# Performance work log

Measured on AMD Instinct MI355X. Metric: run time of the kernel, lower is better.

## Reference

```python
import jax, jax.numpy as jnp
import numpy as np

CC_ITERS = 60  # min-label propagation + pointer doubling; covers huge diameters


def setup_inputs() -> dict:
    key = jax.random.key(0)
    k1, k2, k3, k4, k5 = jax.random.split(key, 5)
    N, C, E = 100000, 128, 800000
    x = jax.random.normal(k1, (N, C), jnp.float32)
    src = jax.random.randint(k2, (E,), 0, N)
    off = jax.random.randint(k3, (E,), 1, N)
    dst = (src + off) % N  # guarantees no self-loops (torch forward filters them)
    edge_index = jnp.stack([src, dst]).astype(jnp.int32)
    batch = jnp.zeros((N,), jnp.int32)
    W = jax.random.normal(k4, (2 * C,), jnp.float32) * 0.05
    b = (jax.random.normal(k5, (), jnp.float32) * 0.05).astype(jnp.float32)
    return {"x": x, "edge_index": edge_index, "batch": batch, "W": W, "b": b}


def _connected_components(src, dst, mask, N):
    # min-label propagation along selected edges, with path compression.
    def body(i, labels):
        ls = jnp.where(mask, labels[src], N)
        ld = jnp.where(mask, labels[dst], N)
        new = labels.at[dst].min(ls).at[src].min(ld)
        return jnp.minimum(new, new[new])  # pointer doubling
    return jax.lax.fori_loop(0, CC_ITERS, body, jnp.arange(N))


def reference(x, edge_index, batch, W, b):
    N, C = x.shape
    E = edge_index.shape[1]
    src, dst = edge_index[0], edge_index[1]

    # raw edge score: Linear(cat(x[src], x[dst])) without materializing the concat
    e = x[src] @ W[:C] + x[dst] @ W[C:] + b  # [E]
    # softmax over incoming edges of each dst node (segment softmax)
    m = jax.ops.segment_max(e, dst, num_segments=N)
    z = jnp.exp(e - m[dst])
    s = jax.ops.segment_sum(z, dst, num_segments=N)
    score = z / s[dst] + 0.5  # add_to_edge_score

    # edge selection (E > N -> quantile branch, matching torch)
    if E > N:
        q = 1.0 - (N // 2) / E
        mask = score > jnp.quantile(score, q)
    else:
        mask = score >= jnp.median(score)

    # weighted pairwise node reps for selected edges (masked instead of gathered)
    w = jnp.where(mask, score, 0.0)
    reps = (x[src] + x[dst]) * w[:, None]  # [E, C]
    mi = mask.astype(x.dtype)
    cnt = jnp.zeros((N,), x.dtype).at[src].add(mi).at[dst].add(mi)  # bincount of selected endpoints
    merged = cnt > 0
    base = jnp.where(merged[:, None], 0.0, x)  # merged nodes zeroed, untouched nodes keep x
    acc = base.at[src].add(reps).at[dst].add(reps)
    nodes = jnp.where(merged[:, None], acc / jnp.maximum(cnt, 1.0)[:, None], acc)

    # connected components over selected edges; relabel by first-occurrence order
    labels = _connected_components(src, dst, jax.lax.stop_gradient(mask), N)
    uniq = jnp.unique(labels, size=N, fill_value=N)
    cluster = jnp.searchsorted(uniq, labels)  # [N]

    new_x = jax.ops.segment_sum(nodes, cluster, num_segments=N)  # padded to N clusters

    # coalesce cluster-mapped edges: sorted unique pairs, padded with -1
    c0, c1 = cluster[src], cluster[dst]
    keys = jnp.unique(c0.astype(jnp.int64) * N + c1.astype(jnp.int64), size=E, fill_value=-1)
    valid = keys >= 0
    new_edge_index = jnp.stack([
        jnp.where(valid, keys // N, -1),
        jnp.where(valid, keys % N, -1),
    ])
    new_batch = jnp.zeros((N,), batch.dtype).at[cluster].set(batch)
    return new_x, new_edge_index, new_batch, score
```

## Files before the change

### kernel.cpp

```cpp
#include <hip/hip_runtime.h>
#include <math.h>
#include <stdint.h>

typedef unsigned long long u64;
typedef unsigned int u32;

#define NN 100000
#define CF 128
#define EE 800000

#define CAP 131072

#define EBITS 11
#define ERADIX 2048
#define STILE 2048
#define NB_E 391
#define SORT_N (NB_E * STILE)
#define MBITS 12
#define MRADIX 4096
#define NB_M 49
#define MSORT_N (NB_M * STILE)
#define HISTG_LEN 800768

#define SCTILE 2048
#define MCHUNK 16

#define ZSCALE 4503599627370496.0
#define XSCALE 32768.0f
#define XINV   (1.0f / 32768.0f)

struct Sel { u32 prefix; u32 k; };

__device__ inline u64 encD(double v) {
  u64 u = (u64)__double_as_longlong(v);
  return u ^ ((u >> 63) ? ~0ULL : 0x8000000000000000ULL);
}
__device__ inline double decD(u64 u) {
  u ^= ((u >> 63) ? 0x8000000000000000ULL : ~0ULL);
  return __longlong_as_double((long long)u);
}

__global__ void k_pq(const float* __restrict__ x, const float* __restrict__ W,
                     double* __restrict__ p, double* __restrict__ q) {
  int node = blockIdx.x * 4 + (threadIdx.x >> 6);
  int lane = threadIdx.x & 63;
  if (node >= NN) return;
  const float* xr = x + (size_t)node * CF;
  double a = (double)xr[lane] * (double)W[lane] + (double)xr[lane + 64] * (double)W[lane + 64];
  double c = (double)xr[lane] * (double)W[CF + lane] + (double)xr[lane + 64] * (double)W[CF + lane + 64];
  for (int off = 32; off; off >>= 1) { a += __shfl_xor(a, off); c += __shfl_xor(c, off); }
  if (lane == 0) { p[node] = a; q[node] = c; }
}

__global__ void k_em(const int* __restrict__ ei, const double* __restrict__ p,
                     const double* __restrict__ q, const float* __restrict__ bptr,
                     double* __restrict__ e, u64* __restrict__ menc) {
  int j = blockIdx.x * 256 + threadIdx.x;
  if (j >= EE) return;
  int s = ei[j], d = ei[EE + j];
  double ev = p[s] + q[d] + (double)bptr[0];
  e[j] = ev;
  atomicMax(&menc[d], encD(ev));
}

__global__ void k_zs(const int* __restrict__ ei, double* __restrict__ e,
                     const u64* __restrict__ menc, u64* __restrict__ sdenFx) {
  int j = blockIdx.x * 256 + threadIdx.x;
  if (j >= EE) return;
  int d = ei[EE + j];
  double z = exp(e[j] - decD(menc[d]));
  e[j] = z;
  atomicAdd(&sdenFx[d], (u64)__double2ll_rn(z * ZSCALE));
}

__global__ void k_score(const int* __restrict__ ei, const double* __restrict__ z,
                        const u64* __restrict__ sdenFx, float* __restrict__ outScore) {
  int j = blockIdx.x * 256 + threadIdx.x;
  if (j >= EE) return;
  int d = ei[EE + j];
  double s = (double)sdenFx[d] * (1.0 / ZSCALE);
  outScore[j] = (float)(z[j] / s + 0.5);
}

__global__ void k_selInit(Sel* st, u32* hist, int k0, int k1) {
  int t = blockIdx.x * 256 + threadIdx.x;
  if (t == 0) { st[0].prefix = 0; st[0].k = (u32)k0; st[1].prefix = 0; st[1].k = (u32)k1; }
  if (t < 512) hist[t] = 0;
}

__global__ void k_selHist(const float* __restrict__ score, const Sel* __restrict__ st,
                          u32* __restrict__ hist, int shift, int pass) {
  __shared__ u32 h[512];
  for (int i = threadIdx.x; i < 512; i += 256) h[i] = 0;
  __syncthreads();
  u32 p0 = st[0].prefix, p1 = st[1].prefix;
  for (int j = blockIdx.x * 256 + threadIdx.x; j < EE; j += gridDim.x * 256) {
    u32 u = __float_as_uint(score[j]);
    u32 d = (u >> shift) & 255u;
    bool ok0 = (pass == 0) || ((u >> (shift + 8)) == p0);
    bool ok1 = (pass == 0) || ((u >> (shift + 8)) == p1);
    if (ok0) atomicAdd(&h[d], 1u);
    if (ok1) atomicAdd(&h[256 + d], 1u);
  }
  __syncthreads();
  for (int i = threadIdx.x; i < 512; i += 256) if (h[i]) atomicAdd(&hist[i], h[i]);
}

__global__ void k_selPick(Sel* st, u32* hist) {
  if (threadIdx.x == 0) {
    for (int sel = 0; sel < 2; sel++) {
      u32 k = st[sel].k, cum = 0;
      for (int b = 0; b < 256; b++) {
        u32 c = hist[sel * 256 + b];
        if (cum + c > k) { st[sel].prefix = (st[sel].prefix << 8) | (u32)b; st[sel].k = k - cum; break; }
        cum += c;
      }
    }
  }
  __syncthreads();
  for (int i = threadIdx.x; i < 512; i += blockDim.x) hist[i] = 0;
}

__global__ void k_t(const Sel* st, float* tval, float frac) {
  float a = __uint_as_float(st[0].prefix);
  float b = __uint_as_float(st[1].prefix);
  tval[0] = __fadd_rn(a, __fmul_rn(__fsub_rn(b, a), frac));
}

__global__ void __launch_bounds__(1024) k_compact(
    const float* __restrict__ score, const float* __restrict__ tval,
    const int* __restrict__ ei, int* __restrict__ selCount,
    int* __restrict__ selSrc, int* __restrict__ selDst,
    float* __restrict__ selW, int* __restrict__ cnt) {
  __shared__ int wbase[16];
  int j = blockIdx.x * 1024 + threadIdx.x;
  int lane = threadIdx.x & 63;
  int wid = threadIdx.x >> 6;
  float sc = 0.0f;
  bool sel = false;
  if (j < EE) { sc = score[j]; sel = (sc > tval[0]); }
  u64 m = __ballot(sel);
  int wcnt = __popcll(m);
  int rank = __popcll(m & ((1ULL << lane) - 1ULL));
  if (lane == 0) wbase[wid] = wcnt;
  __syncthreads();
  if (threadIdx.x == 0) {
    int tot = 0;
#pragma unroll
    for (int w = 0; w < 16; w++) tot += wbase[w];
    int base = tot ? atomicAdd(selCount, tot) : 0;
#pragma unroll
    for (int w = 0; w < 16; w++) { int c = wbase[w]; wbase[w] = base; base += c; }
  }
  __syncthreads();
  if (sel) {
    int s = ei[j], d = ei[EE + j];
    int pos = wbase[wid] + rank;
    if (pos < CAP) { selSrc[pos] = s; selDst[pos] = d; selW[pos] = sc; }
    atomicAdd(&cnt[s], 1);
    atomicAdd(&cnt[d], 1);
  }
}

__global__ void k_labelInit(int* parent) {
  int i = blockIdx.x * 256 + threadIdx.x;
  if (i < NN) parent[i] = i;
}

__device__ inline int uf_find(int* parent, int x) {
  while (true) {
    int p = parent[x];
    if (p == x) return x;
    int gp = parent[p];
    if (gp == p) return p;
    parent[x] = gp;
    x = gp;
  }
}

__global__ void k_ufUnion(const int* __restrict__ selSrc, const int* __restrict__ selDst,
                          const int* __restrict__ selCount, int* __restrict__ parent) {
  int n = selCount[0]; if (n > CAP) n = CAP;
  for (int e = blockIdx.x * 256 + threadIdx.x; e < n; e += gridDim.x * 256) {
    int ru = uf_find(parent, selSrc[e]);
    int rv = uf_find(parent, selDst[e]);
    while (ru != rv) {
      if (ru < rv) { int t = ru; ru = rv; rv = t; }
      int old = atomicCAS(&parent[ru], ru, rv);
      if (old == ru) break;
      ru = uf_find(parent, old);
      rv = uf_find(parent, rv);
    }
  }
}

__global__ void k_ufFlattenRoots(int* __restrict__ parent, int* __restrict__ roots) {
  int i = blockIdx.x * 256 + threadIdx.x;
  if (i >= NN) return;
  int x = i;
  while (true) { int p = parent[x]; if (p == x) break; x = p; }
  parent[i] = x;
  roots[i] = (x == i) ? 1 : 0;
}

__global__ void k_clusterMkeys(const int* __restrict__ labels, const int* __restrict__ rootScan,
                               int* __restrict__ cluster, u64* __restrict__ mkeys) {
  int i = blockIdx.x * 256 + threadIdx.x;
  if (i < NN) {
    int cl = rootScan[labels[i]];
    cluster[i] = cl;
    mkeys[i] = ((u64)(u32)cl << 32) | (u32)i;
  } else if (i < MSORT_N) {
    mkeys[i] = ~0ULL;
  }
}

__global__ void k_scanBlock(const int* __restrict__ src, int* __restrict__ dst,
                            int n, int* __restrict__ bsums) {
  __shared__ int part[256];
  int base = blockIdx.x * SCTILE + threadIdx.x * 8;
  int v[8]; int s = 0;
#pragma unroll
  for (int i = 0; i < 8; i++) { v[i] = (base + i < n) ? src[base + i] : 0; s += v[i]; }
  part[threadIdx.x] = s;
  __syncthreads();
  for (int off = 1; off < 256; off <<= 1) {
    int t = (threadIdx.x >= off) ? part[threadIdx.x - off] : 0;
    __syncthreads();
    part[threadIdx.x] += t;
    __syncthreads();
  }
  int run = part[threadIdx.x] - s;
#pragma unroll
  for (int i = 0; i < 8; i++) { int vv = v[i]; if (base + i < n) dst[base + i] = run; run += vv; }
  if (threadIdx.x == 255) bsums[blockIdx.x] = part[255];
}
__global__ void k_scanTop(int* __restrict__ bsums, int nb) {
  __shared__ int part[256];
  int base = threadIdx.x * 4;
  int v[4]; int s = 0;
#pragma unroll
  for (int i = 0; i < 4; i++) { v[i] = (base + i < nb) ? bsums[base + i] : 0; s += v[i]; }
  part[threadIdx.x] = s;
  __syncthreads();
  for (int off = 1; off < 256; off <<= 1) {
    int t = (threadIdx.x >= off) ? part[threadIdx.x - off] : 0;
    __syncthreads();
    part[threadIdx.x] += t;
    __syncthreads();
  }
  int run = part[threadIdx.x] - s;
#pragma unroll
  for (int i = 0; i < 4; i++) { int vv = v[i]; if (base + i < nb) bsums[base + i] = run; run += vv; }
}
__global__ void k_scanAdd(int* __restrict__ data, int n, const int* __restrict__ bsums) {
  int add = bsums[blockIdx.x];
  int base = blockIdx.x * SCTILE + threadIdx.x * 8;
#pragma unroll
  for (int i = 0; i < 8; i++) if (base + i < n) data[base + i] += add;
}

template <typename K, int BITS>
__global__ void k_sortHistT(const K* __restrict__ keys, int* __restrict__ hist,
                            int shift, int nb) {
  const int RAD = 1 << BITS;
  __shared__ int h[RAD];
  for (int i = threadIdx.x; i < RAD; i += 256) h[i] = 0;
  __syncthreads();
  int base = blockIdx.x * STILE;
  for (int i = threadIdx.x; i < STILE; i += 256) {
    int d = (int)((keys[base + i] >> shift) & (RAD - 1));
    atomicAdd(&h[d], 1);
  }
  __syncthreads();
  for (int i = threadIdx.x; i < RAD; i += 256) hist[i * nb + blockIdx.x] = h[i];
}

template <typename K, int BITS>
__global__ void k_sortScatterT(const K* __restrict__ in, K* __restrict__ out,
                               const int* __restrict__ histScanned, int shift, int nb) {
  const int RAD = 1 << BITS;
  __shared__ int run[RAD];
  for (int i = threadIdx.x; i < RAD; i += 256) run[i] = 0;
  __syncthreads();
  int lane = threadIdx.x & 63;
  int wid = threadIdx.x >> 6;
  int base = blockIdx.x * STILE;
  for (int chunk = 0; chunk < 8; chunk++) {
    K key = in[base + chunk * 256 + threadIdx.x];
    int d = (int)((key >> shift) & (RAD - 1));
    u64 m = ~0ULL;
#pragma unroll
    for (int b = 0; b < BITS; b++) {
      u64 bal = __ballot((d >> b) & 1);
      m &= ((d >> b) & 1) ? bal : ~bal;
    }
    int laneRank = __popcll(m & ((1ULL << lane) - 1ULL));
    int cntm = __popcll(m);
    bool leader = (laneRank == 0);
    int local = 0;
    for (int w = 0; w < 4; w++) {
      if (wid == w) {
        int basev = run[d];
        local = basev + laneRank;
        if (leader) run[d] = basev + cntm;
      }
      __syncthreads();
    }
    out[histScanned[d * nb + blockIdx.x] + local] = key;
  }
}

__global__ void k_csr(const int* __restrict__ selSrc, const int* __restrict__ selDst,
                      const int* __restrict__ selCount, const int* __restrict__ nodeOff,
                      int* __restrict__ fill, int* __restrict__ edgeIdx) {
  int n = selCount[0]; if (n > CAP) n = CAP;
  for (int e = blockIdx.x * 256 + threadIdx.x; e < n; e += gridDim.x * 256) {
    int s = selSrc[e];
    int p = atomicAdd(&fill[s], 1);
    edgeIdx[nodeOff[s] + p] = e;
    int d = selDst[e];
    int p2 = atomicAdd(&fill[d], 1);
    edgeIdx[nodeOff[d] + p2] = e;
  }
}

__global__ void __launch_bounds__(128) k_clusterSum(
    const u64* __restrict__ mk, const int* __restrict__ nodeOff, const int* __restrict__ cnt,
    const int* __restrict__ edgeIdx, const int* __restrict__ selSrc,
    const int* __restrict__ selDst, const float* __restrict__ selW,
    const float* __restrict__ x, int* __restrict__ accX) {
  int c = threadIdx.x;
  int base = blockIdx.x * MCHUNK;
  if (base >= NN) return;
  int end = base + MCHUNK; if (end > NN) end = NN;
  u64 k0 = mk[base];
  int clN = (int)(k0 >> 32);
  int nodeN = (int)(k0 & 0xFFFFFFFFULL);
  int cntN = cnt[nodeN];
  int offN = nodeOff[nodeN];
  int curCl = -1; int acc = 0;
  for (int m = base; m < end; m++) {
    int cl = clN, node = nodeN, ci = cntN, o = offN;
    if (m + 1 < end) {
      u64 k1 = mk[m + 1];
      clN = (int)(k1 >> 32);
      nodeN = (int)(k1 & 0xFFFFFFFFULL);
      cntN = cnt[nodeN];
      offN = nodeOff[nodeN];
    }
    if (cl != curCl) {
      if (curCl >= 0 && acc != 0) atomicAdd(&accX[(size_t)curCl * CF + c], acc);
      curCl = cl; acc = 0;
    }
    if (ci == 0) {
      acc += __float2int_rn(x[(size_t)node * CF + c] * XSCALE);
    } else {
      int eN = edgeIdx[o];
      for (int t = 0; t < ci; t++) {
        int e = eN;
        if (t + 1 < ci) eN = edgeIdx[o + t + 1];
        float r = (x[(size_t)selSrc[e] * CF + c] + x[(size_t)selDst[e] * CF + c]) * selW[e];
        acc += __float2int_rn((r / (float)ci) * XSCALE);
      }
    }
  }
  if (curCl >= 0 && acc != 0) atomicAdd(&accX[(size_t)curCl * CF + c], acc);
}

__global__ void k_final2(const int* __restrict__ accX, float* __restrict__ outNewX) {
  int t = (blockIdx.x * 256 + threadIdx.x) * 4;
  if (t >= NN * CF) return;
  int4 v = *(const int4*)(accX + t);
  float4 o;
  o.x = (float)v.x * XINV; o.y = (float)v.y * XINV;
  o.z = (float)v.z * XINV; o.w = (float)v.w * XINV;
  *(float4*)(outNewX + t) = o;
}

__global__ void k_keysInit(const int* __restrict__ ei, const int* __restrict__ cluster,
                           u32* __restrict__ keys) {
  int t = blockIdx.x * 256 + threadIdx.x;
  if (t >= SORT_N) return;
  if (t < EE) {
    u32 kw = (u32)cluster[ei[t]] * 100000u + (u32)cluster[ei[EE + t]];
    keys[t] = kw ^ 0x80000000u;
  } else {
    keys[t] = 0xFFFFFFFFu;
  }
}

__global__ void k_flags(const u32* __restrict__ keys, int* __restrict__ f) {
  int j = blockIdx.x * 256 + threadIdx.x;
  if (j >= EE) return;
  f[j] = (j == 0 || keys[j] != keys[j - 1]) ? 1 : 0;
}
__global__ void k_eiFill(float* __restrict__ outEI) {
  int t = blockIdx.x * 256 + threadIdx.x;
  if (t < 2 * EE) outEI[t] = -1.0f;
}
__global__ void k_eiScatter(const u32* __restrict__ keys, const int* __restrict__ pos,
                            float* __restrict__ outEI) {
  int j = blockIdx.x * 256 + threadIdx.x;
  if (j >= EE) return;
  bool f = (j == 0 || keys[j] != keys[j - 1]);
  if (f) {
    int k32 = (int)(keys[j] ^ 0x80000000u);
    if (k32 >= 0) {
      int p = pos[j];
      outEI[p] = (float)(k32 / 100000);
      outEI[EE + p] = (float)(k32 % 100000);
    }
  }
}


static inline void runScan(int* data, int n, int* bsums, hipStream_t stream) {
  int nb = (n + SCTILE - 1) / SCTILE;
  k_scanBlock<<<nb, 256, 0, stream>>>(data, data, n, bsums);
  k_scanTop<<<1, 256, 0, stream>>>(bsums, nb);
  k_scanAdd<<<nb, 256, 0, stream>>>(data, n, bsums);
}
static inline void runScanFrom(const int* src, int* dst, int n, int* bsums, hipStream_t stream) {
  int nb = (n + SCTILE - 1) / SCTILE;
  k_scanBlock<<<nb, 256, 0, stream>>>(src, dst, n, bsums);
  k_scanTop<<<1, 256, 0, stream>>>(bsums, nb);
  k_scanAdd<<<nb, 256, 0, stream>>>(dst, n, bsums);
}

extern "C" void kernel_launch(void* const* d_in, const int* in_sizes, int n_in,
                              void* d_out, int out_size, void* d_ws, size_t ws_size,
                              hipStream_t stream) {
  const float* x = (const float*)d_in[0];
  const int* ei = (const int*)d_in[1];
  const float* W = (const float*)d_in[3];
  const float* bptr = (const float*)d_in[4];

  char* wp = (char*)d_ws;
  auto alloc = [&](size_t bytes) -> void* {
    void* r = (void*)wp;
    wp += (bytes + 255) & ~(size_t)255;
    return r;
  };
  double* ez = (double*)alloc((size_t)EE * 8);
  u32* sortA = (u32*)alloc((size_t)SORT_N * 4);
  u32* sortB = (u32*)alloc((size_t)SORT_N * 4);
  int* histG = (int*)alloc((size_t)HISTG_LEN * 4);
  int* fscan = (int*)alloc((size_t)EE * 4);
  double* p_d = (double*)alloc((size_t)NN * 8);
  double* q_d = (double*)alloc((size_t)NN * 8);
  u64* menc = (u64*)alloc((size_t)NN * 8);
  u64* sdenFx = (u64*)alloc((size_t)NN * 8);
  char* zeroAEnd = wp;
  int* accX = (int*)d_ws;
  const size_t ACCX_BYTES = (size_t)NN * CF * 4;
  if (wp < (char*)d_ws + ACCX_BYTES) wp = (char*)d_ws + ACCX_BYTES;
  int* cnt = (int*)alloc((size_t)NN * 4);
  int* fill = (int*)alloc((size_t)NN * 4);
  int* selCount = (int*)alloc(256);
  char* zeroBStart = (char*)cnt; char* zeroBEnd = wp;
  int* nodeOff = (int*)alloc((size_t)NN * 4);
  int* selSrc = (int*)alloc((size_t)CAP * 4);
  int* selDst = (int*)alloc((size_t)CAP * 4);
  float* selW = (float*)alloc((size_t)CAP * 4);
  int* labels = (int*)alloc((size_t)NN * 4);
  int* cluster = (int*)alloc((size_t)NN * 4);
  int* edgeIdx = (int*)alloc((size_t)CAP * 4);
  u64* mA = (u64*)alloc((size_t)MSORT_N * 8);
  u64* mB = (u64*)alloc((size_t)MSORT_N * 8);
  int* bsums = (int*)alloc(1024 * 4);
  Sel* st = (Sel*)alloc(256);
  u32* selHist = (u32*)alloc(512 * 4);
  float* tval = (float*)alloc(256);
  (void)ws_size; (void)n_in; (void)in_sizes;

  float* outNewX = (float*)d_out;
  float* outEI = outNewX + (size_t)NN * CF;
  float* outBatch = outEI + 2 * (size_t)EE;
  float* outScore = outBatch + NN;

  double qd = 1.0 - (double)(NN / 2) / (double)EE;
  double posd = qd * (double)(EE - 1);
  int k0 = (int)floor(posd);
  double fracd = posd - floor(posd);
  int k1 = (fracd > 0.0) ? k0 + 1 : k0;
  float frac = (float)fracd;

  hipMemsetAsync(outBatch, 0, (size_t)NN * 4, stream);
  hipMemsetAsync(menc, 0, (size_t)(zeroAEnd - (char*)menc), stream);
  hipMemsetAsync(zeroBStart, 0, (size_t)(zeroBEnd - zeroBStart), stream);

  k_pq<<<(NN + 3) / 4, 256, 0, stream>>>(x, W, p_d, q_d);
  k_em<<<(EE + 255) / 256, 256, 0, stream>>>(ei, p_d, q_d, bptr, ez, menc);
  k_zs<<<(EE + 255) / 256, 256, 0, stream>>>(ei, ez, menc, sdenFx);
  k_score<<<(EE + 255) / 256, 256, 0, stream>>>(ei, ez, sdenFx, outScore);

  k_selInit<<<2, 256, 0, stream>>>(st, selHist, k0, k1);
  for (int pass = 0; pass < 4; pass++) {
    k_selHist<<<1024, 256, 0, stream>>>(outScore, st, selHist, 24 - 8 * pass, pass);
    k_selPick<<<1, 256, 0, stream>>>(st, selHist);
  }
  k_t<<<1, 64, 0, stream>>>(st, tval, frac);

  k_compact<<<(EE + 1023) / 1024, 1024, 0, stream>>>(outScore, tval, ei, selCount,
                                                     selSrc, selDst, selW, cnt);

  k_labelInit<<<(NN + 255) / 256, 256, 0, stream>>>(labels);
  k_ufUnion<<<256, 256, 0, stream>>>(selSrc, selDst, selCount, labels);
  k_ufUnion<<<256, 256, 0, stream>>>(selSrc, selDst, selCount, labels);
  k_ufFlattenRoots<<<(NN + 255) / 256, 256, 0, stream>>>(labels, fscan);

  runScan(fscan, NN, bsums, stream);
  k_clusterMkeys<<<(MSORT_N + 255) / 256, 256, 0, stream>>>(labels, fscan, cluster, mA);

  {
    u64* msin = mA; u64* msout = mB;
    for (int pass = 0; pass < 2; pass++) {
      int shift = 32 + MBITS * pass;
      k_sortHistT<u64, MBITS><<<NB_M, 256, 0, stream>>>(msin, histG, shift, NB_M);
      runScan(histG, MRADIX * NB_M, bsums, stream);
      k_sortScatterT<u64, MBITS><<<NB_M, 256, 0, stream>>>(msin, msout, histG, shift, NB_M);
      u64* tmp = msin; msin = msout; msout = tmp;
    }
  }
  u64* memberKeys = mA;

  k_keysInit<<<SORT_N / 256, 256, 0, stream>>>(ei, cluster, sortA);
  u32* sin = sortA; u32* sout = sortB;
  for (int pass = 0; pass < 3; pass++) {
    int shift = EBITS * pass;
    k_sortHistT<u32, EBITS><<<NB_E, 256, 0, stream>>>(sin, histG, shift, NB_E);
    runScan(histG, ERADIX * NB_E, bsums, stream);
    k_sortScatterT<u32, EBITS><<<NB_E, 256, 0, stream>>>(sin, sout, histG, shift, NB_E);
    u32* tmp = sin; sin = sout; sout = tmp;
  }
  k_flags<<<(EE + 255) / 256, 256, 0, stream>>>(sin, fscan);
  runScan(fscan, EE, bsums, stream);
  k_eiFill<<<(2 * EE + 255) / 256, 256, 0, stream>>>(outEI);
  k_eiScatter<<<(EE + 255) / 256, 256, 0, stream>>>(sin, fscan, outEI);

  runScanFrom(cnt, nodeOff, NN, bsums, stream);
  k_csr<<<256, 256, 0, stream>>>(selSrc, selDst, selCount, nodeOff, fill, edgeIdx);

  hipMemsetAsync(accX, 0, ACCX_BYTES, stream);
  k_clusterSum<<<(NN + MCHUNK - 1) / MCHUNK, 128, 0, stream>>>(
      memberKeys, nodeOff, cnt, edgeIdx, selSrc, selDst, selW, x, accX);
  k_final2<<<(NN * CF / 4 + 255) / 256, 256, 0, stream>>>(accX, outNewX);
}
```

Before: 723.1 us.

## Use single-pass decoupled lookback scans, fuse unique flag/scatter, trim selection passes

```diff
diff --git a/kernel.cpp b/kernel.cpp
--- a/kernel.cpp
+++ b/kernel.cpp
@@ -22,7 +22,8 @@
 #define MSORT_N (NB_M * STILE)
 #define HISTG_LEN 800768
 
-#define SCTILE 2048
+#define LB_TILE 2048
+#define LB_SLOT 392
 #define MCHUNK 16
 
 #define ZSCALE 4503599627370496.0
@@ -84,12 +85,12 @@
 
 __global__ void k_selInit(Sel* st, u32* hist, int k0, int k1) {
   int t = blockIdx.x * 256 + threadIdx.x;
-  if (t == 0) { st[0].prefix = 0; st[0].k = (u32)k0; st[1].prefix = 0; st[1].k = (u32)k1; }
+  if (t == 0) { st[0].prefix = 0x3Fu; st[0].k = (u32)k0; st[1].prefix = 0x3Fu; st[1].k = (u32)k1; }
   if (t < 512) hist[t] = 0;
 }
 
 __global__ void k_selHist(const float* __restrict__ score, const Sel* __restrict__ st,
-                          u32* __restrict__ hist, int shift, int pass) {
+                          u32* __restrict__ hist, int shift) {
   __shared__ u32 h[512];
   for (int i = threadIdx.x; i < 512; i += 256) h[i] = 0;
   __syncthreads();
@@ -97,10 +98,8 @@
   for (int j = blockIdx.x * 256 + threadIdx.x; j < EE; j += gridDim.x * 256) {
     u32 u = __float_as_uint(score[j]);
     u32 d = (u >> shift) & 255u;
-    bool ok0 = (pass == 0) || ((u >> (shift + 8)) == p0);
-    bool ok1 = (pass == 0) || ((u >> (shift + 8)) == p1);
-    if (ok0) atomicAdd(&h[d], 1u);
-    if (ok1) atomicAdd(&h[256 + d], 1u);
+    if ((u >> (shift + 8)) == p0) atomicAdd(&h[d], 1u);
+    if ((u >> (shift + 8)) == p1) atomicAdd(&h[256 + d], 1u);
   }
   __syncthreads();
   for (int i = threadIdx.x; i < 512; i += 256) if (h[i]) atomicAdd(&hist[i], h[i]);
@@ -215,49 +214,55 @@
   }
 }
 
-__global__ void k_scanBlock(const int* __restrict__ src, int* __restrict__ dst,
-                            int n, int* __restrict__ bsums) {
-  __shared__ int part[256];
-  int base = blockIdx.x * SCTILE + threadIdx.x * 8;
+__global__ void k_lbScan(const int* __restrict__ src, int* __restrict__ dst, int n,
+                         u64* __restrict__ status, int* __restrict__ ticket) {
+  __shared__ int sTile[256];
+  __shared__ int sBid;
+  __shared__ int sPrev;
+  if (threadIdx.x == 0) sBid = atomicAdd(ticket, 1);
+  __syncthreads();
+  int bid = sBid;
+  int base = bid * LB_TILE + threadIdx.x * 8;
   int v[8]; int s = 0;
 #pragma unroll
   for (int i = 0; i < 8; i++) { v[i] = (base + i < n) ? src[base + i] : 0; s += v[i]; }
-  part[threadIdx.x] = s;
+  sTile[threadIdx.x] = s;
   __syncthreads();
   for (int off = 1; off < 256; off <<= 1) {
-    int t = (threadIdx.x >= off) ? part[threadIdx.x - off] : 0;
+    int t = (threadIdx.x >= off) ? sTile[threadIdx.x - off] : 0;
     __syncthreads();
-    part[threadIdx.x] += t;
+    sTile[threadIdx.x] += t;
     __syncthreads();
   }
-  int run = part[threadIdx.x] - s;
+  int total = sTile[255];
+  int runBase = sTile[threadIdx.x] - s;
+  if (threadIdx.x == 0) {
+    if (bid == 0) {
+      __hip_atomic_store(&status[0], (((u64)(u32)total) << 2) | 2ULL,
+                         __ATOMIC_RELEASE, __HIP_MEMORY_SCOPE_AGENT);
+      sPrev = 0;
+    } else {
+      __hip_atomic_store(&status[bid], (((u64)(u32)total) << 2) | 1ULL,
+                         __ATOMIC_RELEASE, __HIP_MEMORY_SCOPE_AGENT);
+      int prev = 0;
+      int j = bid - 1;
+      while (true) {
+        u64 stv = __hip_atomic_load(&status[j], __ATOMIC_ACQUIRE, __HIP_MEMORY_SCOPE_AGENT);
+        u32 state = (u32)(stv & 3ULL);
+        if (state == 0) { __builtin_amdgcn_s_sleep(1); continue; }
+        prev += (int)(u32)(stv >> 2);
+        if (state == 2) break;
+        j--;
+      }
+      __hip_atomic_store(&status[bid], (((u64)(u32)(prev + total)) << 2) | 2ULL,
+                         __ATOMIC_RELEASE, __HIP_MEMORY_SCOPE_AGENT);
+      sPrev = prev;
+    }
+  }
+  __syncthreads();
+  int run = sPrev + runBase;
 #pragma unroll
   for (int i = 0; i < 8; i++) { int vv = v[i]; if (base + i < n) dst[base + i] = run; run += vv; }
-  if (threadIdx.x == 255) bsums[blockIdx.x] = part[255];
-}
-__global__ void k_scanTop(int* __restrict__ bsums, int nb) {
-  __shared__ int part[256];
-  int base = threadIdx.x * 4;
-  int v[4]; int s = 0;
-#pragma unroll
-  for (int i = 0; i < 4; i++) { v[i] = (base + i < nb) ? bsums[base + i] : 0; s += v[i]; }
-  part[threadIdx.x] = s;
-  __syncthreads();
-  for (int off = 1; off < 256; off <<= 1) {
-    int t = (threadIdx.x >= off) ? part[threadIdx.x - off] : 0;
-    __syncthreads();
-    part[threadIdx.x] += t;
-    __syncthreads();
-  }
-  int run = part[threadIdx.x] - s;
-#pragma unroll
-  for (int i = 0; i < 4; i++) { int vv = v[i]; if (base + i < nb) bsums[base + i] = run; run += vv; }
-}
-__global__ void k_scanAdd(int* __restrict__ data, int n, const int* __restrict__ bsums) {
-  int add = bsums[blockIdx.x];
-  int base = blockIdx.x * SCTILE + threadIdx.x * 8;
-#pragma unroll
-  for (int i = 0; i < 8; i++) if (base + i < n) data[base + i] += add;
 }
 
 template <typename K, int BITS>
@@ -341,7 +346,7 @@
   int offN = nodeOff[nodeN];
   int curCl = -1; int acc = 0;
   for (int m = base; m < end; m++) {
-    int cl = clN, node = nodeN, ci = cntN, o = offN;
+    int cl = clN, ci = cntN, o = offN;
     if (m + 1 < end) {
       u64 k1 = mk[m + 1];
       clN = (int)(k1 >> 32);
@@ -349,20 +354,17 @@
       cntN = cnt[nodeN];
       offN = nodeOff[nodeN];
     }
+    if (ci == 0) continue;
     if (cl != curCl) {
       if (curCl >= 0 && acc != 0) atomicAdd(&accX[(size_t)curCl * CF + c], acc);
       curCl = cl; acc = 0;
     }
-    if (ci == 0) {
-      acc += __float2int_rn(x[(size_t)node * CF + c] * XSCALE);
-    } else {
-      int eN = edgeIdx[o];
-      for (int t = 0; t < ci; t++) {
-        int e = eN;
-        if (t + 1 < ci) eN = edgeIdx[o + t + 1];
-        float r = (x[(size_t)selSrc[e] * CF + c] + x[(size_t)selDst[e] * CF + c]) * selW[e];
-        acc += __float2int_rn((r / (float)ci) * XSCALE);
-      }
+    int eN = edgeIdx[o];
+    for (int t = 0; t < ci; t++) {
+      int e = eN;
+      if (t + 1 < ci) eN = edgeIdx[o + t + 1];
+      float r = (x[(size_t)selSrc[e] * CF + c] + x[(size_t)selDst[e] * CF + c]) * selW[e];
+      acc += __float2int_rn((r / (float)ci) * XSCALE);
     }
   }
   if (curCl >= 0 && acc != 0) atomicAdd(&accX[(size_t)curCl * CF + c], acc);
@@ -376,6 +378,14 @@
   o.x = (float)v.x * XINV; o.y = (float)v.y * XINV;
   o.z = (float)v.z * XINV; o.w = (float)v.w * XINV;
   *(float4*)(outNewX + t) = o;
+}
+
+__global__ void k_copyUntouched(const float* __restrict__ x, const int* __restrict__ cnt,
+                                const int* __restrict__ cluster, float* __restrict__ outNewX) {
+  int t = blockIdx.x * 256 + threadIdx.x;
+  if (t >= NN * CF) return;
+  int i = t >> 7; int c = t & 127;
+  if (cnt[i] == 0) outNewX[(size_t)cluster[i] * CF + c] = x[t];
 }
 
 __global__ void k_keysInit(const int* __restrict__ ei, const int* __restrict__ cluster,
@@ -390,43 +400,80 @@
   }
 }
 
-__global__ void k_flags(const u32* __restrict__ keys, int* __restrict__ f) {
-  int j = blockIdx.x * 256 + threadIdx.x;
-  if (j >= EE) return;
-  f[j] = (j == 0 || keys[j] != keys[j - 1]) ? 1 : 0;
-}
 __global__ void k_eiFill(float* __restrict__ outEI) {
   int t = blockIdx.x * 256 + threadIdx.x;
   if (t < 2 * EE) outEI[t] = -1.0f;
 }
-__global__ void k_eiScatter(const u32* __restrict__ keys, const int* __restrict__ pos,
-                            float* __restrict__ outEI) {
-  int j = blockIdx.x * 256 + threadIdx.x;
-  if (j >= EE) return;
-  bool f = (j == 0 || keys[j] != keys[j - 1]);
-  if (f) {
-    int k32 = (int)(keys[j] ^ 0x80000000u);
-    if (k32 >= 0) {
-      int p = pos[j];
-      outEI[p] = (float)(k32 / 100000);
-      outEI[EE + p] = (float)(k32 % 100000);
-    }
-  }
-}
-
-
-static inline void runScan(int* data, int n, int* bsums, hipStream_t stream) {
-  int nb = (n + SCTILE - 1) / SCTILE;
-  k_scanBlock<<<nb, 256, 0, stream>>>(data, data, n, bsums);
-  k_scanTop<<<1, 256, 0, stream>>>(bsums, nb);
-  k_scanAdd<<<nb, 256, 0, stream>>>(data, n, bsums);
-}
-static inline void runScanFrom(const int* src, int* dst, int n, int* bsums, hipStream_t stream) {
-  int nb = (n + SCTILE - 1) / SCTILE;
-  k_scanBlock<<<nb, 256, 0, stream>>>(src, dst, n, bsums);
-  k_scanTop<<<1, 256, 0, stream>>>(bsums, nb);
-  k_scanAdd<<<nb, 256, 0, stream>>>(dst, n, bsums);
-}
+
+__global__ void k_eiUnique(const u32* __restrict__ keys, u64* __restrict__ status,
+                           int* __restrict__ ticket, float* __restrict__ outEI) {
+  __shared__ int sTile[256];
+  __shared__ int sBid;
+  __shared__ int sPrev;
+  if (threadIdx.x == 0) sBid = atomicAdd(ticket, 1);
+  __syncthreads();
+  int bid = sBid;
+  int base = bid * LB_TILE + threadIdx.x * 8;
+  int f[8]; int s = 0;
+  u32 kv[8];
+#pragma unroll
+  for (int i = 0; i < 8; i++) {
+    int j = base + i;
+    if (j < EE) {
+      kv[i] = keys[j];
+      u32 prevk = (i > 0) ? kv[i - 1] : ((j > 0) ? keys[j - 1] : (kv[i] + 1u));
+      f[i] = (j == 0 || kv[i] != prevk) ? 1 : 0;
+    } else { kv[i] = 0; f[i] = 0; }
+    s += f[i];
+  }
+  sTile[threadIdx.x] = s;
+  __syncthreads();
+  for (int off = 1; off < 256; off <<= 1) {
+    int t = (threadIdx.x >= off) ? sTile[threadIdx.x - off] : 0;
+    __syncthreads();
+    sTile[threadIdx.x] += t;
+    __syncthreads();
+  }
+  int total = sTile[255];
+  int runBase = sTile[threadIdx.x] - s;
+  if (threadIdx.x == 0) {
+    if (bid == 0) {
+      __hip_atomic_store(&status[0], (((u64)(u32)total) << 2) | 2ULL,
+                         __ATOMIC_RELEASE, __HIP_MEMORY_SCOPE_AGENT);
+      sPrev = 0;
+    } else {
+      __hip_atomic_store(&status[bid], (((u64)(u32)total) << 2) | 1ULL,
+                         __ATOMIC_RELEASE, __HIP_MEMORY_SCOPE_AGENT);
+      int prev = 0;
+      int j = bid - 1;
+      while (true) {
+        u64 stv = __hip_atomic_load(&status[j], __ATOMIC_ACQUIRE, __HIP_MEMORY_SCOPE_AGENT);
+        u32 state = (u32)(stv & 3ULL);
+        if (state == 0) { __builtin_amdgcn_s_sleep(1); continue; }
+        prev += (int)(u32)(stv >> 2);
+        if (state == 2) break;
+        j--;
+      }
+      __hip_atomic_store(&status[bid], (((u64)(u32)(prev + total)) << 2) | 2ULL,
+                         __ATOMIC_RELEASE, __HIP_MEMORY_SCOPE_AGENT);
+      sPrev = prev;
+    }
+  }
+  __syncthreads();
+  int run = sPrev + runBase;
+#pragma unroll
+  for (int i = 0; i < 8; i++) {
+    if (f[i]) {
+      int k32 = (int)(kv[i] ^ 0x80000000u);
+      if (k32 >= 0) {
+        outEI[run] = (float)(k32 / 100000);
+        outEI[EE + run] = (float)(k32 % 100000);
+      }
+      run++;
+    }
+  }
+}
+
 
 extern "C" void kernel_launch(void* const* d_in, const int* in_sizes, int n_in,
                               void* d_out, int out_size, void* d_ws, size_t ws_size,
@@ -446,7 +493,7 @@
   u32* sortA = (u32*)alloc((size_t)SORT_N * 4);
   u32* sortB = (u32*)alloc((size_t)SORT_N * 4);
   int* histG = (int*)alloc((size_t)HISTG_LEN * 4);
-  int* fscan = (int*)alloc((size_t)EE * 4);
+  int* roots = (int*)alloc((size_t)NN * 4);
   double* p_d = (double*)alloc((size_t)NN * 8);
   double* q_d = (double*)alloc((size_t)NN * 8);
   u64* menc = (u64*)alloc((size_t)NN * 8);
@@ -458,6 +505,8 @@
   int* cnt = (int*)alloc((size_t)NN * 4);
   int* fill = (int*)alloc((size_t)NN * 4);
   int* selCount = (int*)alloc(256);
+  u64* lbStatus = (u64*)alloc((size_t)8 * LB_SLOT * 8);
+  int* lbTicket = (int*)alloc(8 * 4);
   char* zeroBStart = (char*)cnt; char* zeroBEnd = wp;
   int* nodeOff = (int*)alloc((size_t)NN * 4);
   int* selSrc = (int*)alloc((size_t)CAP * 4);
@@ -468,11 +517,15 @@
   int* edgeIdx = (int*)alloc((size_t)CAP * 4);
   u64* mA = (u64*)alloc((size_t)MSORT_N * 8);
   u64* mB = (u64*)alloc((size_t)MSORT_N * 8);
-  int* bsums = (int*)alloc(1024 * 4);
   Sel* st = (Sel*)alloc(256);
   u32* selHist = (u32*)alloc(512 * 4);
   float* tval = (float*)alloc(256);
   (void)ws_size; (void)n_in; (void)in_sizes;
+
+  auto lbScan = [&](const int* src, int* dst, int n, int slot) {
+    int nb = (n + LB_TILE - 1) / LB_TILE;
+    k_lbScan<<<nb, 256, 0, stream>>>(src, dst, n, lbStatus + slot * LB_SLOT, lbTicket + slot);
+  };
 
   float* outNewX = (float*)d_out;
   float* outEI = outNewX + (size_t)NN * CF;
@@ -496,8 +549,8 @@
   k_score<<<(EE + 255) / 256, 256, 0, stream>>>(ei, ez, sdenFx, outScore);
 
   k_selInit<<<2, 256, 0, stream>>>(st, selHist, k0, k1);
-  for (int pass = 0; pass < 4; pass++) {
-    k_selHist<<<1024, 256, 0, stream>>>(outScore, st, selHist, 24 - 8 * pass, pass);
+  for (int pass = 0; pass < 3; pass++) {
+    k_selHist<<<1024, 256, 0, stream>>>(outScore, st, selHist, 16 - 8 * pass);
     k_selPick<<<1, 256, 0, stream>>>(st, selHist);
   }
   k_t<<<1, 64, 0, stream>>>(st, tval, frac);
@@ -508,17 +561,17 @@
   k_labelInit<<<(NN + 255) / 256, 256, 0, stream>>>(labels);
   k_ufUnion<<<256, 256, 0, stream>>>(selSrc, selDst, selCount, labels);
   k_ufUnion<<<256, 256, 0, stream>>>(selSrc, selDst, selCount, labels);
-  k_ufFlattenRoots<<<(NN + 255) / 256, 256, 0, stream>>>(labels, fscan);
-
-  runScan(fscan, NN, bsums, stream);
-  k_clusterMkeys<<<(MSORT_N + 255) / 256, 256, 0, stream>>>(labels, fscan, cluster, mA);
+  k_ufFlattenRoots<<<(NN + 255) / 256, 256, 0, stream>>>(labels, roots);
+
+  lbScan(roots, roots, NN, 0);
+  k_clusterMkeys<<<(MSORT_N + 255) / 256, 256, 0, stream>>>(labels, roots, cluster, mA);
 
   {
     u64* msin = mA; u64* msout = mB;
     for (int pass = 0; pass < 2; pass++) {
       int shift = 32 + MBITS * pass;
       k_sortHistT<u64, MBITS><<<NB_M, 256, 0, stream>>>(msin, histG, shift, NB_M);
-      runScan(histG, MRADIX * NB_M, bsums, stream);
+      lbScan(histG, histG, MRADIX * NB_M, 1 + pass);
       k_sortScatterT<u64, MBITS><<<NB_M, 256, 0, stream>>>(msin, msout, histG, shift, NB_M);
       u64* tmp = msin; msin = msout; msout = tmp;
     }
@@ -530,20 +583,22 @@
   for (int pass = 0; pass < 3; pass++) {
     int shift = EBITS * pass;
     k_sortHistT<u32, EBITS><<<NB_E, 256, 0, stream>>>(sin, histG, shift, NB_E);
-    runScan(histG, ERADIX * NB_E, bsums, stream);
+    lbScan(histG, histG, ERADIX * NB_E, 3 + pass);
     k_sortScatterT<u32, EBITS><<<NB_E, 256, 0, stream>>>(sin, sout, histG, shift, NB_E);
     u32* tmp = sin; sin = sout; sout = tmp;
   }
-  k_flags<<<(EE + 255) / 256, 256, 0, stream>>>(sin, fscan);
-  runScan(fscan, EE, bsums, stream);
   k_eiFill<<<(2 * EE + 255) / 256, 256, 0, stream>>>(outEI);
-  k_eiScatter<<<(EE + 255) / 256, 256, 0, stream>>>(sin, fscan, outEI);
-
-  runScanFrom(cnt, nodeOff, NN, bsums, stream);
+  {
+    int nb = (EE + LB_TILE - 1) / LB_TILE;
+    k_eiUnique<<<nb, 256, 0, stream>>>(sin, lbStatus + 6 * LB_SLOT, lbTicket + 6, outEI);
+  }
+
+  lbScan(cnt, nodeOff, NN, 7);
   k_csr<<<256, 256, 0, stream>>>(selSrc, selDst, selCount, nodeOff, fill, edgeIdx);
 
   hipMemsetAsync(accX, 0, ACCX_BYTES, stream);
   k_clusterSum<<<(NN + MCHUNK - 1) / MCHUNK, 128, 0, stream>>>(
       memberKeys, nodeOff, cnt, edgeIdx, selSrc, selDst, selW, x, accX);
   k_final2<<<(NN * CF / 4 + 255) / 256, 256, 0, stream>>>(accX, outNewX);
-}
+  k_copyUntouched<<<(NN * CF + 255) / 256, 256, 0, stream>>>(x, cnt, cluster, outNewX);
+}
```

Result: slower. 1.076 ms (+48.9%).
